# Performance work log

Hardware: AMD Instinct MI355X
Metric: run time of the kernel (lower is better)

The kernel has to match this reference:

```python
import jax, jax.numpy as jnp
import numpy as np

N_ENTITIES = 100000
N_EDGES = 500000
N_RELATIONS = 200
DIM = 64
HEADS = 4
POW_ITER = 5
ALPHA = 0.1
LEAKY_SLOPE = 0.01
EPS = 1e-16


def setup_inputs() -> dict:
    key = jax.random.key(0)
    ks = jax.random.split(key, 11)
    scale = 0.1
    return {
        "entity_embed": jax.random.normal(ks[0], (N_ENTITIES, DIM), jnp.float32),
        "relation_embed": jax.random.normal(ks[1], (N_RELATIONS, DIM), jnp.float32),
        "W_h": jax.random.normal(ks[2], (DIM, HEADS * DIM), jnp.float32) * scale,
        "W_t": jax.random.normal(ks[3], (DIM, HEADS * DIM), jnp.float32) * scale,
        "W_r": jax.random.normal(ks[4], (DIM, HEADS * DIM), jnp.float32) * scale,
        "att_h": jax.random.normal(ks[5], (HEADS, DIM), jnp.float32) * scale,
        "att_t": jax.random.normal(ks[6], (HEADS, DIM), jnp.float32) * scale,
        "att_r": jax.random.normal(ks[7], (HEADS, DIM), jnp.float32) * scale,
        "W_o": jax.random.normal(ks[8], (HEADS * DIM, DIM), jnp.float32) * scale,
        "edge_index": jax.random.randint(ks[9], (2, N_EDGES), 0, N_ENTITIES, jnp.int64),
        "edge_type": jax.random.randint(ks[10], (N_EDGES,), 0, N_RELATIONS, jnp.int64),
    }


def _segment_softmax(scores, seg_ids, num_segments):
    # scores: [E, heads]; softmax over edges sharing the same seg_id, per head
    m = jax.ops.segment_max(scores, seg_ids, num_segments=num_segments)
    e = jnp.exp(scores - m[seg_ids])
    denom = jax.ops.segment_sum(e, seg_ids, num_segments=num_segments)
    return e / (denom[seg_ids] + EPS)


def reference(entity_embed, relation_embed, W_h, W_t, W_r,
              att_h, att_t, att_r, W_o, edge_index, edge_type):
    head_ids, tail_ids = edge_index[0], edge_index[1]

    # per-edge gathered embeddings, projected per head: [E, heads, dim]
    Wh = (entity_embed[head_ids] @ W_h).reshape(-1, HEADS, DIM)
    Wt = (entity_embed[tail_ids] @ W_t).reshape(-1, HEADS, DIM)
    Wr = (relation_embed[edge_type] @ W_r).reshape(-1, HEADS, DIM)

    s_h = jnp.sum(jnp.tanh(Wh) * att_h[None], axis=-1)  # [E, heads]
    s_t = jnp.sum(jnp.tanh(Wt) * att_t[None], axis=-1)
    s_r = jnp.sum(jnp.tanh(Wr) * att_r[None], axis=-1)
    scores = jax.nn.leaky_relu(s_h + s_t + s_r, negative_slope=LEAKY_SLOPE)

    att = _segment_softmax(scores, head_ids, N_ENTITIES)  # [E, heads]
    A = (1.0 - ALPHA) * att

    # PPR power iteration, vectorized over heads: Z: [N, heads, dim]
    Z0 = entity_embed[:, None, :]  # [N, 1, dim]
    Z_init = jnp.broadcast_to(Z0, (N_ENTITIES, HEADS, DIM))

    def step(Z, _):
        msgs = A[:, :, None] * Z[tail_ids]  # [E, heads, dim]
        Z_new = jax.ops.segment_sum(msgs, head_ids, num_segments=N_ENTITIES) + ALPHA * Z0
        return Z_new, None

    Z, _ = jax.lax.scan(step, Z_init, None, length=POW_ITER)

    out = Z.reshape(N_ENTITIES, HEADS * DIM) @ W_o  # [N, dim]
    return out
```

## Files before the change

kernel.cpp:

```cpp
#include <hip/hip_runtime.h>
#include <hip/hip_fp16.h>
#include <math.h>

#define N_ENT 100000
#define N_EDGE 500000
#define N_REL 200

typedef short bf16x8 __attribute__((ext_vector_type(8)));
typedef _Float16 f16x8 __attribute__((ext_vector_type(8)));
typedef float f32x4 __attribute__((ext_vector_type(4)));

__device__ __forceinline__ float fast_tanh(float x) {
    float xc = fminf(x, 15.f);
    float e = __expf(2.f * xc);
    return 1.f - 2.f * __builtin_amdgcn_rcpf(e + 1.f);
}

__device__ __forceinline__ unsigned short f2bf(float f) {
    unsigned u = __float_as_uint(f);
    unsigned r = u + 0x7FFF + ((u >> 16) & 1);
    return (unsigned short)(r >> 16);
}

__device__ __forceinline__ uint2 pack_half4(const float4 v) {
    __half2 lo = __floats2half2_rn(v.x, v.y);
    __half2 hi = __floats2half2_rn(v.z, v.w);
    uint2 r;
    r.x = *reinterpret_cast<const unsigned int*>(&lo);
    r.y = *reinterpret_cast<const unsigned int*>(&hi);
    return r;
}

__device__ __forceinline__ float4 unpack_half4(uint2 u) {
    __half2 lo = *reinterpret_cast<const __half2*>(&u.x);
    __half2 hi = *reinterpret_cast<const __half2*>(&u.y);
    float2 a = __half22float2(lo);
    float2 b = __half22float2(hi);
    return make_float4(a.x, a.y, b.x, b.y);
}

#define HIST_B 1954
#define EMB_B  2048
#define WT_B   128
#define WOT_B  64
__global__ __launch_bounds__(256) void prep_kernel(
    const float* __restrict__ entity, unsigned short* __restrict__ emb_bf,
    const float* __restrict__ W0, const float* __restrict__ W1,
    unsigned short* __restrict__ wT,
    const float* __restrict__ Wo, __half* __restrict__ woT,
    const int* __restrict__ eidx, int* __restrict__ counts)
{
    int bid = blockIdx.x;
    if (bid < HIST_B) {
        int e = bid * 256 + threadIdx.x;
        if (e < N_EDGE) atomicAdd(&counts[eidx[e]], 1);
    } else if (bid < HIST_B + EMB_B) {
        int b = bid - HIST_B;
        const int nquads = N_ENT * 64 / 4;
        for (int i = b * 256 + threadIdx.x; i < nquads; i += EMB_B * 256) {
            float4 v = ((const float4*)entity)[i];
            ushort4 o;
            o.x = f2bf(v.x); o.y = f2bf(v.y); o.z = f2bf(v.z); o.w = f2bf(v.w);
            ((ushort4*)emb_bf)[i] = o;
        }
    } else if (bid < HIST_B + EMB_B + WT_B) {
        int idx = (bid - HIST_B - EMB_B) * 256 + threadIdx.x;
        int mat = idx >> 14;
        int rem = idx & 16383;
        int col = rem >> 6;
        int k   = rem & 63;
        const float* W = (mat == 0) ? W0 : W1;
        wT[idx] = f2bf(W[k * 256 + col]);
    } else {
        int idx = (bid - HIST_B - EMB_B - WT_B) * 256 + threadIdx.x;
        int d = idx >> 8;
        int k = idx & 255;
        woT[idx] = __float2half(Wo[k * 64 + d]);
    }
}

__global__ __launch_bounds__(256) void proj_mfma_kernel(
    const unsigned short* __restrict__ emb_bf,
    const unsigned short* __restrict__ wT,
    const float* __restrict__ att0, const float* __restrict__ att1,
    float* __restrict__ p0, float* __restrict__ p1, int nrows, int nb)
{
    const int mat = (blockIdx.x >= nb) ? 1 : 0;
    const int rb  = blockIdx.x - mat * nb;
    const float* att = (mat == 0) ? att0 : att1;
    float* p         = (mat == 0) ? p0 : p1;
    const unsigned short* wbase = wT + (size_t)mat * 256 * 64;

    const int wv   = threadIdx.x >> 6;
    const int lane = threadIdx.x & 63;
    const int r4   = lane >> 4;
    const int cl   = lane & 15;
    const int rowbase = rb * 64 + wv * 16;

    int ra = min(rowbase + cl, nrows - 1);
    bf16x8 a0 = *(const bf16x8*)(emb_bf + (size_t)ra * 64 + 8 * r4);
    bf16x8 a1 = *(const bf16x8*)(emb_bf + (size_t)ra * 64 + 8 * r4 + 32);

    float pacc[4][4];
#pragma unroll
    for (int head = 0; head < 4; ++head) {
        float vsum[4] = {0.f, 0.f, 0.f, 0.f};
#pragma unroll
        for (int sub = 0; sub < 4; ++sub) {
            int col = head * 64 + sub * 16 + cl;
            const unsigned short* wp = wbase + (size_t)col * 64 + 8 * r4;
            bf16x8 b0 = *(const bf16x8*)(wp);
            bf16x8 b1 = *(const bf16x8*)(wp + 32);
            f32x4 c = {0.f, 0.f, 0.f, 0.f};
            c = __builtin_amdgcn_mfma_f32_16x16x32_bf16(a0, b0, c, 0, 0, 0);
            c = __builtin_amdgcn_mfma_f32_16x16x32_bf16(a1, b1, c, 0, 0, 0);
            float av = att[head * 64 + sub * 16 + cl];
#pragma unroll
            for (int j = 0; j < 4; ++j)
                vsum[j] = fmaf(fast_tanh(c[j]), av, vsum[j]);
        }
#pragma unroll
        for (int j = 0; j < 4; ++j) {
            float v = vsum[j];
            v += __shfl_xor(v, 1, 64);
            v += __shfl_xor(v, 2, 64);
            v += __shfl_xor(v, 4, 64);
            v += __shfl_xor(v, 8, 64);
            pacc[head][j] = v;
        }
    }
    if (cl == 0) {
#pragma unroll
        for (int j = 0; j < 4; ++j) {
            int row = rowbase + r4 * 4 + j;
            if (row < nrows) {
                *(float4*)(p + (size_t)row * 4) = make_float4(
                    pacc[0][j], pacc[1][j], pacc[2][j], pacc[3][j]);
            }
        }
    }
}

__global__ __launch_bounds__(256) void proj_gemm_kernel(
    const float* __restrict__ emb,
    const float* __restrict__ W0,
    const float* __restrict__ att0,
    float* __restrict__ p0,
    int nrows)
{
    __shared__ float e_lds[64][68];
    __shared__ float w0_lds[64][64];
    __shared__ float red[4][4][64];

    const int t    = threadIdx.x;
    const int wv   = t >> 6;
    const int lane = t & 63;
    const int er   = t & 15;
    const int d0   = (t >> 4) * 4;
    const int base = blockIdx.x * 64;

#pragma unroll
    for (int i = 0; i < 4; ++i) {
        int f = t + 256 * i;
        int row = f >> 4, c4 = f & 15;
        int gr = min(base + row, nrows - 1);
        float4 v = *(const float4*)(emb + (size_t)gr * 64 + 4 * c4);
        *(float4*)&e_lds[row][4 * c4] = v;
    }

    float p0s[4][4];

    for (int head = 0; head < 4; ++head) {
        {
            int k0 = t >> 4, c4 = t & 15;
#pragma unroll
            for (int kk = 0; kk < 4; ++kk) {
                int k = k0 + 16 * kk;
                *(float4*)&w0_lds[k][4 * c4] =
                    *(const float4*)(W0 + (size_t)k * 256 + head * 64 + 4 * c4);
            }
        }
        __syncthreads();

        float acc0[4][4] = {};
        for (int k4 = 0; k4 < 16; ++k4) {
            float4 z0 = *(const float4*)&e_lds[er +  0][4 * k4];
            float4 z1 = *(const float4*)&e_lds[er + 16][4 * k4];
            float4 z2 = *(const float4*)&e_lds[er + 32][4 * k4];
            float4 z3 = *(const float4*)&e_lds[er + 48][4 * k4];
            const float zr[4][4] = {
                {z0.x, z0.y, z0.z, z0.w},
                {z1.x, z1.y, z1.z, z1.w},
                {z2.x, z2.y, z2.z, z2.w},
                {z3.x, z3.y, z3.z, z3.w}};
#pragma unroll
            for (int jj = 0; jj < 4; ++jj) {
                float4 w0v = *(const float4*)&w0_lds[4 * k4 + jj][d0];
#pragma unroll
                for (int i = 0; i < 4; ++i) {
                    float zj = zr[i][jj];
                    acc0[i][0] = fmaf(zj, w0v.x, acc0[i][0]);
                    acc0[i][1] = fmaf(zj, w0v.y, acc0[i][1]);
                    acc0[i][2] = fmaf(zj, w0v.z, acc0[i][2]);
                    acc0[i][3] = fmaf(zj, w0v.w, acc0[i][3]);
                }
            }
        }

        float4 av0 = *(const float4*)(att0 + head * 64 + d0);
#pragma unroll
        for (int i = 0; i < 4; ++i) {
            float v = fast_tanh(acc0[i][0]) * av0.x
                    + fast_tanh(acc0[i][1]) * av0.y
                    + fast_tanh(acc0[i][2]) * av0.z
                    + fast_tanh(acc0[i][3]) * av0.w;
            v += __shfl_xor(v, 16, 64);
            v += __shfl_xor(v, 32, 64);
            p0s[head][i] = v;
        }
        __syncthreads();
    }

    if (lane < 16) {
#pragma unroll
        for (int h = 0; h < 4; ++h)
#pragma unroll
            for (int i = 0; i < 4; ++i)
                red[wv][h][lane + 16 * i] = p0s[h][i];
    }
    __syncthreads();
    if (t < 64) {
        int row = base + t;
        if (row < nrows) {
            float4 pv;
            pv.x = red[0][0][t] + red[1][0][t] + red[2][0][t] + red[3][0][t];
            pv.y = red[0][1][t] + red[1][1][t] + red[2][1][t] + red[3][1][t];
            pv.z = red[0][2][t] + red[1][2][t] + red[2][2][t] + red[3][2][t];
            pv.w = red[0][3][t] + red[1][3][t] + red[2][3][t] + red[3][3][t];
            *(float4*)(p0 + (size_t)row * 4) = pv;
        }
    }
}

__global__ __launch_bounds__(1024) void scan_kernel(
    const int* __restrict__ counts, int* __restrict__ row_start)
{
    __shared__ int wsum[16];
    __shared__ int carry_s;
    const int lane = threadIdx.x & 63;
    const int wid  = threadIdx.x >> 6;
    if (threadIdx.x == 0) carry_s = 0;
    __syncthreads();
    for (int base = 0; base < N_ENT; base += 4096) {
        int i0 = base + (int)threadIdx.x * 4;
        int4 v = make_int4(0, 0, 0, 0);
        if (i0 + 3 < N_ENT) v = *(const int4*)(counts + i0);
        else {
            if (i0 + 0 < N_ENT) v.x = counts[i0 + 0];
            if (i0 + 1 < N_ENT) v.y = counts[i0 + 1];
            if (i0 + 2 < N_ENT) v.z = counts[i0 + 2];
            if (i0 + 3 < N_ENT) v.w = counts[i0 + 3];
        }
        int s1 = v.x + v.y, s2 = s1 + v.z, tsum = s2 + v.w;
        int incl = tsum;
#pragma unroll
        for (int off = 1; off < 64; off <<= 1) {
            int t = __shfl_up(incl, off, 64);
            if (lane >= off) incl += t;
        }
        if (lane == 63) wsum[wid] = incl;
        __syncthreads();
        int wave_off = 0;
#pragma unroll
        for (int w = 0; w < 16; ++w)
            wave_off += (w < wid) ? wsum[w] : 0;
        int carry = carry_s;
        int excl = carry + wave_off + (incl - tsum);
        if (i0 + 3 < N_ENT) {
            *(int4*)(row_start + i0) = make_int4(excl, excl + v.x, excl + s1, excl + s2);
        } else {
            if (i0 + 0 < N_ENT) row_start[i0 + 0] = excl;
            if (i0 + 1 < N_ENT) row_start[i0 + 1] = excl + v.x;
            if (i0 + 2 < N_ENT) row_start[i0 + 2] = excl + s1;
            if (i0 + 3 < N_ENT) row_start[i0 + 3] = excl + s2;
        }
        __syncthreads();
        if (threadIdx.x == 1023) carry_s = carry + wave_off + incl;
    }
    __syncthreads();
    if (threadIdx.x == 0) row_start[N_ENT] = carry_s;
}

__global__ __launch_bounds__(256) void scatter_score_kernel(
    const int* __restrict__ eidx, const int* __restrict__ etype,
    const float* __restrict__ ph, const float* __restrict__ pt,
    const float* __restrict__ pr,
    const int* __restrict__ row_start, int* __restrict__ cursor,
    int* __restrict__ csr_col, float* __restrict__ csr_a)
{
    int e = blockIdx.x * 256 + threadIdx.x;
    if (e >= N_EDGE) return;
    int hn = eidx[e];
    int tn = eidx[N_EDGE + e];
    int r  = etype[e];
    float4 a = *(const float4*)(ph + (size_t)hn * 4);
    float4 b = *(const float4*)(pt + (size_t)tn * 4);
    float4 c = *(const float4*)(pr + (size_t)r * 4);
    float s0 = a.x + b.x + c.x;
    float s1 = a.y + b.y + c.y;
    float s2 = a.z + b.z + c.z;
    float s3 = a.w + b.w + c.w;
    s0 = s0 >= 0.f ? s0 : 0.01f * s0;
    s1 = s1 >= 0.f ? s1 : 0.01f * s1;
    s2 = s2 >= 0.f ? s2 : 0.01f * s2;
    s3 = s3 >= 0.f ? s3 : 0.01f * s3;
    float4 ev = make_float4(__expf(s0), __expf(s1), __expf(s2), __expf(s3));
    int pos = row_start[hn] + atomicAdd(&cursor[hn], 1);
    csr_col[pos] = tn;
    *(float4*)(csr_a + (size_t)pos * 4) = ev;
}

__global__ __launch_bounds__(256) void norm_spmm1_kernel(
    const float* __restrict__ emb,
    const int* __restrict__ row_start, const int* __restrict__ csr_col,
    float* __restrict__ csr_a, __half* __restrict__ Zout)
{
    const int wave = threadIdx.x >> 6;
    const int lane = threadIdx.x & 63;
    const int n = blockIdx.x * 4 + wave;
    const int h = lane >> 4;
    const int s   = row_start[n];
    const int end = row_start[n + 1];
    const int nf  = (end - s) * 4;

    float sum = 0.f;
    for (int f = lane; f < nf; f += 64)
        sum += csr_a[(size_t)s * 4 + f];
#pragma unroll
    for (int off = 4; off < 64; off <<= 1)
        sum += __shfl_xor(sum, off, 64);
    float scale = 0.9f * __builtin_amdgcn_rcpf(sum + 1e-16f);

    const float4* e4 = (const float4*)emb;
    float4 zi = e4[(size_t)n * 16 + (lane & 15)];
    float4 acc0 = make_float4(0.1f * zi.x, 0.1f * zi.y, 0.1f * zi.z, 0.1f * zi.w);
    float4 acc1 = make_float4(0.f, 0.f, 0.f, 0.f);
    float4 acc2 = make_float4(0.f, 0.f, 0.f, 0.f);
    float4 acc3 = make_float4(0.f, 0.f, 0.f, 0.f);

    auto zrow = [&](int c) -> float4 {
        return *(const float4*)(emb + (size_t)c * 64 + 4 * (lane & 15));
    };
    auto fma4 = [](float4& acc, float a, const float4& z) {
        acc.x = fmaf(a, z.x, acc.x);
        acc.y = fmaf(a, z.y, acc.y);
        acc.z = fmaf(a, z.z, acc.z);
        acc.w = fmaf(a, z.w, acc.w);
    };

    for (int b = s; b < end; b += 16) {
        const int nb = min(16, end - b);
        int   cl = (lane < nb) ? csr_col[b + lane] : 0;
        float al = (lane < nb * 4) ? csr_a[(size_t)b * 4 + lane] : 0.f;
        float aln = al * scale;
        if (lane < nb * 4) csr_a[(size_t)b * 4 + lane] = aln;

        int j = 0;
        for (; j + 4 <= nb; j += 4) {
            int c0 = __shfl(cl, j + 0, 64);
            int c1 = __shfl(cl, j + 1, 64);
            int c2 = __shfl(cl, j + 2, 64);
            int c3 = __shfl(cl, j + 3, 64);
            float a0 = __shfl(aln, (j + 0) * 4 + h, 64);
            float a1 = __shfl(aln, (j + 1) * 4 + h, 64);
            float a2 = __shfl(aln, (j + 2) * 4 + h, 64);
            float a3 = __shfl(aln, (j + 3) * 4 + h, 64);
            float4 za = zrow(c0);
            float4 zb = zrow(c1);
            float4 zc = zrow(c2);
            float4 zd = zrow(c3);
            fma4(acc0, a0, za);
            fma4(acc1, a1, zb);
            fma4(acc2, a2, zc);
            fma4(acc3, a3, zd);
        }
        if (j + 0 < nb) {
            int c = __shfl(cl, j + 0, 64);
            float a = __shfl(aln, (j + 0) * 4 + h, 64);
            fma4(acc0, a, zrow(c));
        }
        if (j + 1 < nb) {
            int c = __shfl(cl, j + 1, 64);
            float a = __shfl(aln, (j + 1) * 4 + h, 64);
            fma4(acc1, a, zrow(c));
        }
        if (j + 2 < nb) {
            int c = __shfl(cl, j + 2, 64);
            float a = __shfl(aln, (j + 2) * 4 + h, 64);
            fma4(acc2, a, zrow(c));
        }
    }
    acc0.x += acc1.x + acc2.x + acc3.x;
    acc0.y += acc1.y + acc2.y + acc3.y;
    acc0.z += acc1.z + acc2.z + acc3.z;
    acc0.w += acc1.w + acc2.w + acc3.w;
    *(uint2*)(Zout + (size_t)n * 256 + 4 * lane) = pack_half4(acc0);
}

__device__ __forceinline__ float4 spmm_row_h(
    int n, int lane, int h,
    const __half* __restrict__ Zin_h, const float* __restrict__ emb,
    const int* __restrict__ row_start, const int* __restrict__ csr_col,
    const float* __restrict__ csr_a)
{
    const float4* e4 = (const float4*)emb;
    float4 zi = e4[(size_t)n * 16 + (lane & 15)];
    float4 acc0 = make_float4(0.1f * zi.x, 0.1f * zi.y, 0.1f * zi.z, 0.1f * zi.w);
    float4 acc1 = make_float4(0.f, 0.f, 0.f, 0.f);
    float4 acc2 = make_float4(0.f, 0.f, 0.f, 0.f);
    float4 acc3 = make_float4(0.f, 0.f, 0.f, 0.f);

    const int s   = row_start[n];
    const int end = row_start[n + 1];

    auto zrow = [&](int c) -> float4 {
        uint2 u = *(const uint2*)(Zin_h + (size_t)c * 256 + 4 * lane);
        return unpack_half4(u);
    };
    auto fma4 = [](float4& acc, float a, const float4& z) {
        acc.x = fmaf(a, z.x, acc.x);
        acc.y = fmaf(a, z.y, acc.y);
        acc.z = fmaf(a, z.z, acc.z);
        acc.w = fmaf(a, z.w, acc.w);
    };

    for (int b = s; b < end; b += 16) {
        const int nb = min(16, end - b);
        int   cl = (lane < nb) ? csr_col[b + lane] : 0;
        float al = (lane < nb * 4) ? csr_a[(size_t)b * 4 + lane] : 0.f;

        int j = 0;
        for (; j + 4 <= nb; j += 4) {
            int c0 = __shfl(cl, j + 0, 64);
            int c1 = __shfl(cl, j + 1, 64);
            int c2 = __shfl(cl, j + 2, 64);
            int c3 = __shfl(cl, j + 3, 64);
            float a0 = __shfl(al, (j + 0) * 4 + h, 64);
            float a1 = __shfl(al, (j + 1) * 4 + h, 64);
            float a2 = __shfl(al, (j + 2) * 4 + h, 64);
            float a3 = __shfl(al, (j + 3) * 4 + h, 64);
            float4 za = zrow(c0);
            float4 zb = zrow(c1);
            float4 zc = zrow(c2);
            float4 zd = zrow(c3);
            fma4(acc0, a0, za);
            fma4(acc1, a1, zb);
            fma4(acc2, a2, zc);
            fma4(acc3, a3, zd);
        }
        if (j + 0 < nb) {
            int c = __shfl(cl, j + 0, 64);
            float a = __shfl(al, (j + 0) * 4 + h, 64);
            fma4(acc0, a, zrow(c));
        }
        if (j + 1 < nb) {
            int c = __shfl(cl, j + 1, 64);
            float a = __shfl(al, (j + 1) * 4 + h, 64);
            fma4(acc1, a, zrow(c));
        }
        if (j + 2 < nb) {
            int c = __shfl(cl, j + 2, 64);
            float a = __shfl(al, (j + 2) * 4 + h, 64);
            fma4(acc2, a, zrow(c));
        }
    }
    acc0.x += acc1.x + acc2.x + acc3.x;
    acc0.y += acc1.y + acc2.y + acc3.y;
    acc0.z += acc1.z + acc2.z + acc3.z;
    acc0.w += acc1.w + acc2.w + acc3.w;
    return acc0;
}

__global__ __launch_bounds__(256) void spmm_kernel(
    const __half* __restrict__ Zin, const float* __restrict__ emb,
    const int* __restrict__ row_start, const int* __restrict__ csr_col,
    const float* __restrict__ csr_a, __half* __restrict__ Zout)
{
    const int wave = threadIdx.x >> 6;
    const int lane = threadIdx.x & 63;
    const int n = blockIdx.x * 4 + wave;
    const int h = lane >> 4;
    float4 acc = spmm_row_h(n, lane, h, Zin, emb, row_start, csr_col, csr_a);
    *(uint2*)(Zout + (size_t)n * 256 + 4 * lane) = pack_half4(acc);
}

__global__ __launch_bounds__(256) void spmm_out_fused_kernel(
    const __half* __restrict__ Zin, const float* __restrict__ emb,
    const int* __restrict__ row_start, const int* __restrict__ csr_col,
    const float* __restrict__ csr_a,
    const __half* __restrict__ woT,
    float* __restrict__ out)
{
    __shared__ _Float16 zl[16][264];
    const int wv   = threadIdx.x >> 6;
    const int lane = threadIdx.x & 63;
    const int h    = lane >> 4;
    const int base = blockIdx.x * 16;

#pragma unroll
    for (int rr = 0; rr < 4; ++rr) {
        int n = base + wv * 4 + rr;
        float4 acc = spmm_row_h(n, lane, h, Zin, emb, row_start, csr_col, csr_a);
        *(uint2*)&zl[wv * 4 + rr][4 * lane] = pack_half4(acc);
    }
    __syncthreads();

    const int cl = lane & 15;
    const int r4 = lane >> 4;
    f16x8 a[8];
#pragma unroll
    for (int ks = 0; ks < 8; ++ks)
        a[ks] = *(const f16x8*)&zl[cl][ks * 32 + 8 * r4];

    const _Float16* wcol = (const _Float16*)woT + (size_t)(wv * 16 + cl) * 256 + 8 * r4;
    f32x4 c = {0.f, 0.f, 0.f, 0.f};
#pragma unroll
    for (int ks = 0; ks < 8; ++ks) {
        f16x8 b = *(const f16x8*)(wcol + ks * 32);
        c = __builtin_amdgcn_mfma_f32_16x16x32_f16(a[ks], b, c, 0, 0, 0);
    }
#pragma unroll
    for (int j = 0; j < 4; ++j) {
        int row = base + r4 * 4 + j;
        out[(size_t)row * 64 + wv * 16 + cl] = c[j];
    }
}

extern "C" void kernel_launch(void* const* d_in, const int* in_sizes, int n_in,
                              void* d_out, int out_size, void* d_ws, size_t ws_size,
                              hipStream_t stream)
{
    const float* entity = (const float*)d_in[0];
    const float* rel    = (const float*)d_in[1];
    const float* W_h    = (const float*)d_in[2];
    const float* W_t    = (const float*)d_in[3];
    const float* W_r    = (const float*)d_in[4];
    const float* att_h  = (const float*)d_in[5];
    const float* att_t  = (const float*)d_in[6];
    const float* att_r  = (const float*)d_in[7];
    const float* W_o    = (const float*)d_in[8];
    const int*   eidx   = (const int*)d_in[9];
    const int*   etype  = (const int*)d_in[10];
    float* out = (float*)d_out;

    char* ws = (char*)d_ws;
    size_t off = 0;
    auto alloc = [&](size_t bytes) -> void* {
        void* p = ws + off;
        off += (bytes + 255) & ~(size_t)255;
        return p;
    };
    float* p_h      = (float*)alloc((size_t)N_ENT * 4 * 4);
    float* p_t      = (float*)alloc((size_t)N_ENT * 4 * 4);
    float* p_r      = (float*)alloc((size_t)N_REL * 4 * 4);
    int*   counts   = (int*)alloc((size_t)N_ENT * 4);
    int*   row_start= (int*)alloc(((size_t)N_ENT + 1) * 4);
    int*   cursor   = (int*)alloc((size_t)N_ENT * 4);
    int*   csr_col  = (int*)alloc((size_t)N_EDGE * 4);
    float* csr_a    = (float*)alloc((size_t)N_EDGE * 4 * 4);
    __half* Zh_a    = (__half*)alloc((size_t)N_ENT * 256 * 2);
    __half* Zh_b    = (__half*)alloc((size_t)N_ENT * 256 * 2);
    unsigned short* emb_bf = (unsigned short*)alloc((size_t)N_ENT * 64 * 2);
    unsigned short* wT     = (unsigned short*)alloc((size_t)2 * 256 * 64 * 2);
    __half* woT     = (__half*)alloc((size_t)64 * 256 * 2);

    hipMemsetAsync(counts, 0, (size_t)N_ENT * 4, stream);
    hipMemsetAsync(cursor, 0, (size_t)N_ENT * 4, stream);

    prep_kernel<<<HIST_B + EMB_B + WT_B + WOT_B, 256, 0, stream>>>(
        entity, emb_bf, W_h, W_t, wT, W_o, woT, eidx, counts);

    const int nb = (N_ENT + 63) / 64;
    proj_mfma_kernel<<<2 * nb, 256, 0, stream>>>(
        emb_bf, wT, att_h, att_t, p_h, p_t, N_ENT, nb);
    proj_gemm_kernel<<<(N_REL + 63) / 64, 256, 0, stream>>>(
        rel, W_r, att_r, p_r, N_REL);

    scan_kernel<<<1, 1024, 0, stream>>>(counts, row_start);
    scatter_score_kernel<<<(N_EDGE + 255) / 256, 256, 0, stream>>>(
        eidx, etype, p_h, p_t, p_r, row_start, cursor, csr_col, csr_a);

    norm_spmm1_kernel<<<N_ENT / 4, 256, 0, stream>>>(
        entity, row_start, csr_col, csr_a, Zh_b);
    spmm_kernel<<<N_ENT / 4, 256, 0, stream>>>(Zh_b, entity, row_start, csr_col, csr_a, Zh_a);
    spmm_kernel<<<N_ENT / 4, 256, 0, stream>>>(Zh_a, entity, row_start, csr_col, csr_a, Zh_b);
    spmm_kernel<<<N_ENT / 4, 256, 0, stream>>>(Zh_b, entity, row_start, csr_col, csr_a, Zh_a);
    spmm_out_fused_kernel<<<N_ENT / 16, 256, 0, stream>>>(
        Zh_a, entity, row_start, csr_col, csr_a, woT, out);
}
```

Baseline: 415.9 us.

## Split wave into half-waves processing edge pairs with 8-wide loads; reuse histogram offsets

Measured after the change: 405.0 us. 1.03x faster.

```diff
diff --git a/kernel.cpp b/kernel.cpp
--- a/kernel.cpp
+++ b/kernel.cpp
@@ -22,21 +22,9 @@
     return (unsigned short)(r >> 16);
 }
 
-__device__ __forceinline__ uint2 pack_half4(const float4 v) {
-    __half2 lo = __floats2half2_rn(v.x, v.y);
-    __half2 hi = __floats2half2_rn(v.z, v.w);
-    uint2 r;
-    r.x = *reinterpret_cast<const unsigned int*>(&lo);
-    r.y = *reinterpret_cast<const unsigned int*>(&hi);
-    return r;
-}
-
-__device__ __forceinline__ float4 unpack_half4(uint2 u) {
-    __half2 lo = *reinterpret_cast<const __half2*>(&u.x);
-    __half2 hi = *reinterpret_cast<const __half2*>(&u.y);
-    float2 a = __half22float2(lo);
-    float2 b = __half22float2(hi);
-    return make_float4(a.x, a.y, b.x, b.y);
+__device__ __forceinline__ unsigned pack_half2(float a, float b) {
+    __half2 h = __floats2half2_rn(a, b);
+    return *reinterpret_cast<unsigned*>(&h);
 }
 
 #define HIST_B 1954
@@ -48,12 +36,13 @@
     const float* __restrict__ W0, const float* __restrict__ W1,
     unsigned short* __restrict__ wT,
     const float* __restrict__ Wo, __half* __restrict__ woT,
-    const int* __restrict__ eidx, int* __restrict__ counts)
+    const int* __restrict__ eidx, int* __restrict__ counts,
+    int* __restrict__ eoff)
 {
     int bid = blockIdx.x;
     if (bid < HIST_B) {
         int e = bid * 256 + threadIdx.x;
-        if (e < N_EDGE) atomicAdd(&counts[eidx[e]], 1);
+        if (e < N_EDGE) eoff[e] = atomicAdd(&counts[eidx[e]], 1);
     } else if (bid < HIST_B + EMB_B) {
         int b = bid - HIST_B;
         const int nquads = N_ENT * 64 / 4;
@@ -295,7 +284,7 @@
     const int* __restrict__ eidx, const int* __restrict__ etype,
     const float* __restrict__ ph, const float* __restrict__ pt,
     const float* __restrict__ pr,
-    const int* __restrict__ row_start, int* __restrict__ cursor,
+    const int* __restrict__ row_start, const int* __restrict__ eoff,
     int* __restrict__ csr_col, float* __restrict__ csr_a)
 {
     int e = blockIdx.x * 256 + threadIdx.x;
@@ -315,9 +304,103 @@
     s2 = s2 >= 0.f ? s2 : 0.01f * s2;
     s3 = s3 >= 0.f ? s3 : 0.01f * s3;
     float4 ev = make_float4(__expf(s0), __expf(s1), __expf(s2), __expf(s3));
-    int pos = row_start[hn] + atomicAdd(&cursor[hn], 1);
+    int pos = row_start[hn] + eoff[e];
     csr_col[pos] = tn;
     *(float4*)(csr_a + (size_t)pos * 4) = ev;
+}
+
+template <bool IN_HALF, bool NORM>
+__device__ __forceinline__ void spmm_row_pair(
+    int n, int lane, float scale,
+    const __half* __restrict__ Zin_h, const float* __restrict__ emb,
+    const int* __restrict__ row_start, const int* __restrict__ csr_col,
+    float* __restrict__ csr_a, float acc[8])
+{
+    const int half = lane >> 5;
+    const int j    = lane & 31;
+    const int hd   = j >> 3;
+    const int s    = row_start[n];
+    const int end  = row_start[n + 1];
+
+    {
+        const float* z0p = emb + (size_t)n * 64 + 8 * (j & 7);
+        float4 z0a = *(const float4*)(z0p);
+        float4 z0b = *(const float4*)(z0p + 4);
+        float m = (half == 0) ? 0.1f : 0.f;
+        acc[0] = m * z0a.x; acc[1] = m * z0a.y; acc[2] = m * z0a.z; acc[3] = m * z0a.w;
+        acc[4] = m * z0b.x; acc[5] = m * z0b.y; acc[6] = m * z0b.z; acc[7] = m * z0b.w;
+    }
+    float accB[8] = {0.f, 0.f, 0.f, 0.f, 0.f, 0.f, 0.f, 0.f};
+
+    for (int b = s; b < end; b += 16) {
+        const int nb = min(16, end - b);
+        int   cl = (lane < nb) ? csr_col[b + lane] : 0;
+        float al = (lane < nb * 4) ? csr_a[(size_t)b * 4 + lane] : 0.f;
+        if (NORM) {
+            al *= scale;
+            if (lane < nb * 4) csr_a[(size_t)b * 4 + lane] = al;
+        }
+        for (int e = 0; e < nb; e += 4) {
+            int iA = half ? min(e + 1, nb - 1) : e;
+            int iB = half ? min(e + 3, nb - 1) : min(e + 2, nb - 1);
+            int cA = __shfl(cl, iA, 64);
+            int cB = __shfl(cl, iB, 64);
+            float aA = __shfl(al, iA * 4 + hd, 64);
+            float aB = __shfl(al, iB * 4 + hd, 64);
+            aA = (e + half < nb) ? aA : 0.f;
+            aB = (e + 2 + half < nb) ? aB : 0.f;
+            if (IN_HALF) {
+                f16x8 zA = *(const f16x8*)(Zin_h + (size_t)cA * 256 + 8 * j);
+                f16x8 zB = *(const f16x8*)(Zin_h + (size_t)cB * 256 + 8 * j);
+#pragma unroll
+                for (int k = 0; k < 8; ++k) {
+                    acc[k]  = fmaf(aA, (float)zA[k], acc[k]);
+                    accB[k] = fmaf(aB, (float)zB[k], accB[k]);
+                }
+            } else {
+                int ec = 8 * (j & 7);
+                float4 zA0 = *(const float4*)(emb + (size_t)cA * 64 + ec);
+                float4 zA1 = *(const float4*)(emb + (size_t)cA * 64 + ec + 4);
+                float4 zB0 = *(const float4*)(emb + (size_t)cB * 64 + ec);
+                float4 zB1 = *(const float4*)(emb + (size_t)cB * 64 + ec + 4);
+                acc[0] = fmaf(aA, zA0.x, acc[0]);
+                acc[1] = fmaf(aA, zA0.y, acc[1]);
+                acc[2] = fmaf(aA, zA0.z, acc[2]);
+                acc[3] = fmaf(aA, zA0.w, acc[3]);
+                acc[4] = fmaf(aA, zA1.x, acc[4]);
+                acc[5] = fmaf(aA, zA1.y, acc[5]);
+                acc[6] = fmaf(aA, zA1.z, acc[6]);
+                acc[7] = fmaf(aA, zA1.w, acc[7]);
+                accB[0] = fmaf(aB, zB0.x, accB[0]);
+                accB[1] = fmaf(aB, zB0.y, accB[1]);
+                accB[2] = fmaf(aB, zB0.z, accB[2]);
+                accB[3] = fmaf(aB, zB0.w, accB[3]);
+                accB[4] = fmaf(aB, zB1.x, accB[4]);
+                accB[5] = fmaf(aB, zB1.y, accB[5]);
+                accB[6] = fmaf(aB, zB1.z, accB[6]);
+                accB[7] = fmaf(aB, zB1.w, accB[7]);
+            }
+        }
+    }
+#pragma unroll
+    for (int k = 0; k < 8; ++k) {
+        float v = acc[k] + accB[k];
+        v += __shfl_xor(v, 32, 64);
+        acc[k] = v;
+    }
+}
+
+__device__ __forceinline__ void store_row_h(
+    __half* __restrict__ dst256, int lane, const float acc[8])
+{
+    if (lane < 32) {
+        uint4 o;
+        o.x = pack_half2(acc[0], acc[1]);
+        o.y = pack_half2(acc[2], acc[3]);
+        o.z = pack_half2(acc[4], acc[5]);
+        o.w = pack_half2(acc[6], acc[7]);
+        *(uint4*)(dst256 + 8 * lane) = o;
+    }
 }
 
 __global__ __launch_bounds__(256) void norm_spmm1_kernel(
@@ -328,7 +411,6 @@
     const int wave = threadIdx.x >> 6;
     const int lane = threadIdx.x & 63;
     const int n = blockIdx.x * 4 + wave;
-    const int h = lane >> 4;
     const int s   = row_start[n];
     const int end = row_start[n + 1];
     const int nf  = (end - s) * 4;
@@ -341,177 +423,52 @@
         sum += __shfl_xor(sum, off, 64);
     float scale = 0.9f * __builtin_amdgcn_rcpf(sum + 1e-16f);
 
-    const float4* e4 = (const float4*)emb;
-    float4 zi = e4[(size_t)n * 16 + (lane & 15)];
-    float4 acc0 = make_float4(0.1f * zi.x, 0.1f * zi.y, 0.1f * zi.z, 0.1f * zi.w);
-    float4 acc1 = make_float4(0.f, 0.f, 0.f, 0.f);
-    float4 acc2 = make_float4(0.f, 0.f, 0.f, 0.f);
-    float4 acc3 = make_float4(0.f, 0.f, 0.f, 0.f);
-
-    auto zrow = [&](int c) -> float4 {
-        return *(const float4*)(emb + (size_t)c * 64 + 4 * (lane & 15));
-    };
-    auto fma4 = [](float4& acc, float a, const float4& z) {
-        acc.x = fmaf(a, z.x, acc.x);
-        acc.y = fmaf(a, z.y, acc.y);
-        acc.z = fmaf(a, z.z, acc.z);
-        acc.w = fmaf(a, z.w, acc.w);
-    };
-
-    for (int b = s; b < end; b += 16) {
-        const int nb = min(16, end - b);
-        int   cl = (lane < nb) ? csr_col[b + lane] : 0;
-        float al = (lane < nb * 4) ? csr_a[(size_t)b * 4 + lane] : 0.f;
-        float aln = al * scale;
-        if (lane < nb * 4) csr_a[(size_t)b * 4 + lane] = aln;
-
-        int j = 0;
-        for (; j + 4 <= nb; j += 4) {
-            int c0 = __shfl(cl, j + 0, 64);
-            int c1 = __shfl(cl, j + 1, 64);
-            int c2 = __shfl(cl, j + 2, 64);
-            int c3 = __shfl(cl, j + 3, 64);
-            float a0 = __shfl(aln, (j + 0) * 4 + h, 64);
-            float a1 = __shfl(aln, (j + 1) * 4 + h, 64);
-            float a2 = __shfl(aln, (j + 2) * 4 + h, 64);
-            float a3 = __shfl(aln, (j + 3) * 4 + h, 64);
-            float4 za = zrow(c0);
-            float4 zb = zrow(c1);
-            float4 zc = zrow(c2);
-            float4 zd = zrow(c3);
-            fma4(acc0, a0, za);
-            fma4(acc1, a1, zb);
-            fma4(acc2, a2, zc);
-            fma4(acc3, a3, zd);
-        }
-        if (j + 0 < nb) {
-            int c = __shfl(cl, j + 0, 64);
-            float a = __shfl(aln, (j + 0) * 4 + h, 64);
-            fma4(acc0, a, zrow(c));
-        }
-        if (j + 1 < nb) {
-            int c = __shfl(cl, j + 1, 64);
-            float a = __shfl(aln, (j + 1) * 4 + h, 64);
-            fma4(acc1, a, zrow(c));
-        }
-        if (j + 2 < nb) {
-            int c = __shfl(cl, j + 2, 64);
-            float a = __shfl(aln, (j + 2) * 4 + h, 64);
-            fma4(acc2, a, zrow(c));
-        }
-    }
-    acc0.x += acc1.x + acc2.x + acc3.x;
-    acc0.y += acc1.y + acc2.y + acc3.y;
-    acc0.z += acc1.z + acc2.z + acc3.z;
-    acc0.w += acc1.w + acc2.w + acc3.w;
-    *(uint2*)(Zout + (size_t)n * 256 + 4 * lane) = pack_half4(acc0);
-}
-
-__device__ __forceinline__ float4 spmm_row_h(
-    int n, int lane, int h,
-    const __half* __restrict__ Zin_h, const float* __restrict__ emb,
-    const int* __restrict__ row_start, const int* __restrict__ csr_col,
-    const float* __restrict__ csr_a)
-{
-    const float4* e4 = (const float4*)emb;
-    float4 zi = e4[(size_t)n * 16 + (lane & 15)];
-    float4 acc0 = make_float4(0.1f * zi.x, 0.1f * zi.y, 0.1f * zi.z, 0.1f * zi.w);
-    float4 acc1 = make_float4(0.f, 0.f, 0.f, 0.f);
-    float4 acc2 = make_float4(0.f, 0.f, 0.f, 0.f);
-    float4 acc3 = make_float4(0.f, 0.f, 0.f, 0.f);
-
-    const int s   = row_start[n];
-    const int end = row_start[n + 1];
-
-    auto zrow = [&](int c) -> float4 {
-        uint2 u = *(const uint2*)(Zin_h + (size_t)c * 256 + 4 * lane);
-        return unpack_half4(u);
-    };
-    auto fma4 = [](float4& acc, float a, const float4& z) {
-        acc.x = fmaf(a, z.x, acc.x);
-        acc.y = fmaf(a, z.y, acc.y);
-        acc.z = fmaf(a, z.z, acc.z);
-        acc.w = fmaf(a, z.w, acc.w);
-    };
-
-    for (int b = s; b < end; b += 16) {
-        const int nb = min(16, end - b);
-        int   cl = (lane < nb) ? csr_col[b + lane] : 0;
-        float al = (lane < nb * 4) ? csr_a[(size_t)b * 4 + lane] : 0.f;
-
-        int j = 0;
-        for (; j + 4 <= nb; j += 4) {
-            int c0 = __shfl(cl, j + 0, 64);
-            int c1 = __shfl(cl, j + 1, 64);
-            int c2 = __shfl(cl, j + 2, 64);
-            int c3 = __shfl(cl, j + 3, 64);
-            float a0 = __shfl(al, (j + 0) * 4 + h, 64);
-            float a1 = __shfl(al, (j + 1) * 4 + h, 64);
-            float a2 = __shfl(al, (j + 2) * 4 + h, 64);
-            float a3 = __shfl(al, (j + 3) * 4 + h, 64);
-            float4 za = zrow(c0);
-            float4 zb = zrow(c1);
-            float4 zc = zrow(c2);
-            float4 zd = zrow(c3);
-            fma4(acc0, a0, za);
-            fma4(acc1, a1, zb);
-            fma4(acc2, a2, zc);
-            fma4(acc3, a3, zd);
-        }
-        if (j + 0 < nb) {
-            int c = __shfl(cl, j + 0, 64);
-            float a = __shfl(al, (j + 0) * 4 + h, 64);
-            fma4(acc0, a, zrow(c));
-        }
-        if (j + 1 < nb) {
-            int c = __shfl(cl, j + 1, 64);
-            float a = __shfl(al, (j + 1) * 4 + h, 64);
-            fma4(acc1, a, zrow(c));
-        }
-        if (j + 2 < nb) {
-            int c = __shfl(cl, j + 2, 64);
-            float a = __shfl(al, (j + 2) * 4 + h, 64);
-            fma4(acc2, a, zrow(c));
-        }
-    }
-    acc0.x += acc1.x + acc2.x + acc3.x;
-    acc0.y += acc1.y + acc2.y + acc3.y;
-    acc0.z += acc1.z + acc2.z + acc3.z;
-    acc0.w += acc1.w + acc2.w + acc3.w;
-    return acc0;
+    float acc[8];
+    spmm_row_pair<false, true>(n, lane, scale, nullptr, emb,
+                               row_start, csr_col, csr_a, acc);
+    store_row_h(Zout + (size_t)n * 256, lane, acc);
 }
 
 __global__ __launch_bounds__(256) void spmm_kernel(
     const __half* __restrict__ Zin, const float* __restrict__ emb,
     const int* __restrict__ row_start, const int* __restrict__ csr_col,
-    const float* __restrict__ csr_a, __half* __restrict__ Zout)
+    float* __restrict__ csr_a, __half* __restrict__ Zout)
 {
     const int wave = threadIdx.x >> 6;
     const int lane = threadIdx.x & 63;
     const int n = blockIdx.x * 4 + wave;
-    const int h = lane >> 4;
-    float4 acc = spmm_row_h(n, lane, h, Zin, emb, row_start, csr_col, csr_a);
-    *(uint2*)(Zout + (size_t)n * 256 + 4 * lane) = pack_half4(acc);
+    float acc[8];
+    spmm_row_pair<true, false>(n, lane, 1.f, Zin, emb,
+                               row_start, csr_col, csr_a, acc);
+    store_row_h(Zout + (size_t)n * 256, lane, acc);
 }
 
 __global__ __launch_bounds__(256) void spmm_out_fused_kernel(
     const __half* __restrict__ Zin, const float* __restrict__ emb,
     const int* __restrict__ row_start, const int* __restrict__ csr_col,
-    const float* __restrict__ csr_a,
+    float* __restrict__ csr_a,
     const __half* __restrict__ woT,
     float* __restrict__ out)
 {
     __shared__ _Float16 zl[16][264];
     const int wv   = threadIdx.x >> 6;
     const int lane = threadIdx.x & 63;
-    const int h    = lane >> 4;
     const int base = blockIdx.x * 16;
 
 #pragma unroll
     for (int rr = 0; rr < 4; ++rr) {
         int n = base + wv * 4 + rr;
-        float4 acc = spmm_row_h(n, lane, h, Zin, emb, row_start, csr_col, csr_a);
-        *(uint2*)&zl[wv * 4 + rr][4 * lane] = pack_half4(acc);
+        float acc[8];
+        spmm_row_pair<true, false>(n, lane, 1.f, Zin, emb,
+                                   row_start, csr_col, csr_a, acc);
+        if (lane < 32) {
+            uint4 o;
+            o.x = pack_half2(acc[0], acc[1]);
+            o.y = pack_half2(acc[2], acc[3]);
+            o.z = pack_half2(acc[4], acc[5]);
+            o.w = pack_half2(acc[6], acc[7]);
+            *(uint4*)&zl[wv * 4 + rr][8 * lane] = o;
+        }
     }
     __syncthreads();
 
@@ -565,7 +522,7 @@
     float* p_r      = (float*)alloc((size_t)N_REL * 4 * 4);
     int*   counts   = (int*)alloc((size_t)N_ENT * 4);
     int*   row_start= (int*)alloc(((size_t)N_ENT + 1) * 4);
-    int*   cursor   = (int*)alloc((size_t)N_ENT * 4);
+    int*   eoff     = (int*)alloc((size_t)N_EDGE * 4);
     int*   csr_col  = (int*)alloc((size_t)N_EDGE * 4);
     float* csr_a    = (float*)alloc((size_t)N_EDGE * 4 * 4);
     __half* Zh_a    = (__half*)alloc((size_t)N_ENT * 256 * 2);
@@ -575,10 +532,9 @@
     __half* woT     = (__half*)alloc((size_t)64 * 256 * 2);
 
     hipMemsetAsync(counts, 0, (size_t)N_ENT * 4, stream);
-    hipMemsetAsync(cursor, 0, (size_t)N_ENT * 4, stream);
 
     prep_kernel<<<HIST_B + EMB_B + WT_B + WOT_B, 256, 0, stream>>>(
-        entity, emb_bf, W_h, W_t, wT, W_o, woT, eidx, counts);
+        entity, emb_bf, W_h, W_t, wT, W_o, woT, eidx, counts, eoff);
 
     const int nb = (N_ENT + 63) / 64;
     proj_mfma_kernel<<<2 * nb, 256, 0, stream>>>(
@@ -588,7 +544,7 @@
 
     scan_kernel<<<1, 1024, 0, stream>>>(counts, row_start);
     scatter_score_kernel<<<(N_EDGE + 255) / 256, 256, 0, stream>>>(
-        eidx, etype, p_h, p_t, p_r, row_start, cursor, csr_col, csr_a);
+        eidx, etype, p_h, p_t, p_r, row_start, eoff, csr_col, csr_a);
 
     norm_spmm1_kernel<<<N_ENT / 4, 256, 0, stream>>>(
         entity, row_start, csr_col, csr_a, Zh_b);
```
